# Kernel optimization log

Hardware: AMD Instinct MI355X
Metric: run time of the kernel (lower is better)

Reference implementation:

```python
import jax, jax.numpy as jnp
import numpy as np

EPS = 1e-5

def _bn(x, g, b, axes):
    # training-mode BatchNorm: biased batch stats over `axes`
    mu = jnp.mean(x, axis=axes, keepdims=True)
    var = jnp.var(x, axis=axes, keepdims=True)
    return (x - mu) * jax.lax.rsqrt(var + EPS) * g + b

def setup_inputs() -> dict:
    key = jax.random.key(0)
    ks = jax.random.split(key, 8)
    N, C, T, V = 32, 64, 512, 25
    H, D, BC = 3, 8, 16
    return {
        'x': jax.random.normal(ks[0], (N, C, T, V), jnp.float32),
        'A_topo': jax.random.uniform(ks[1], (H, V, V), jnp.float32),
        'ln_g': jnp.ones((C,), jnp.float32),
        'ln_b': jnp.zeros((C,), jnp.float32),
        'qk_w': jax.random.normal(ks[2], (2 * H * D, C), jnp.float32),
        'qk_b': jnp.zeros((2 * H * D,), jnp.float32),
        'convd_w': jax.random.normal(ks[3], (H, C, C), jnp.float32) * 0.05,
        'convd_b': jnp.zeros((H, C), jnp.float32),
        'sagc_bn_g': jnp.ones((C,), jnp.float32),
        'sagc_bn_b': jnp.zeros((C,), jnp.float32),
        'tcn_w1': jax.random.normal(ks[4], (4, BC, C), jnp.float32) * 0.1,
        'tcn_b1': jnp.zeros((4, BC), jnp.float32),
        'tcn_bn1_g': jnp.ones((4, BC), jnp.float32),
        'tcn_bn1_b': jnp.zeros((4, BC), jnp.float32),
        'tcn_w2': jax.random.normal(ks[5], (2, BC, BC, 5), jnp.float32) * 0.1,
        'tcn_b2': jnp.zeros((2, BC), jnp.float32),
        'tcn_bn2_g': jnp.ones((3, BC), jnp.float32),
        'tcn_bn2_b': jnp.zeros((3, BC), jnp.float32),
    }

def reference(x, A_topo, ln_g, ln_b, qk_w, qk_b, convd_w, convd_b,
              sagc_bn_g, sagc_bn_b, tcn_w1, tcn_b1, tcn_bn1_g, tcn_bn1_b,
              tcn_w2, tcn_b2, tcn_bn2_g, tcn_bn2_b):
    N, C, T, V = x.shape
    H = A_topo.shape[0]
    D = qk_w.shape[0] // (2 * H)
    scale = D ** -0.5

    # ---- SelfAttention ----
    feat = jnp.transpose(x, (0, 2, 3, 1))              # n t v c
    mu = feat.mean(-1, keepdims=True)
    var = feat.var(-1, keepdims=True)
    y = (feat - mu) * jax.lax.rsqrt(var + EPS) * ln_g + ln_b
    qk = y @ qk_w.T + qk_b                             # n t v 2HD
    q, k = jnp.split(qk, 2, axis=-1)
    q = q.reshape(N, T, V, H, D)
    k = k.reshape(N, T, V, H, D)
    dots = jnp.einsum('ntihd,ntjhd->nthij', q, k) * scale
    attn = jax.nn.softmax(dots, axis=-1)               # n t h v v

    # ---- SA_GC ----
    A = attn * A_topo                                  # broadcast (H,V,V)
    z = jnp.einsum('nthij,ntjc->nthic', A, feat)       # per-head A_h @ feature
    sa = jnp.einsum('nthic,hoc->noti', z, convd_w)     # fused per-head 1x1 convs
    sa = sa + convd_b.sum(0)[None, :, None, None]
    sa = _bn(sa, sagc_bn_g[None, :, None, None], sagc_bn_b[None, :, None, None], (0, 2, 3))
    y_gc = jax.nn.relu(sa + x)                         # down = identity (in==out)

    # ---- MultiScale_TemporalConv ----
    pre = jnp.einsum('nctv,koc->nkotv', y_gc, tcn_w1) + tcn_b1[None, :, :, None, None]
    pre = _bn(pre, tcn_bn1_g[None, :, :, None, None], tcn_bn1_b[None, :, :, None, None], (0, 3, 4))
    act = jax.nn.relu(pre[:, :3])                      # branches 0..2 get ReLU
    branches = []
    for i, d in enumerate((1, 2)):                     # dilated temporal convs
        pad = 2 * d                                    # (kernel-1)*d//2
        w = tcn_w2[i][:, :, :, None]                   # (O,I,5,1)
        zb = jax.lax.conv_general_dilated(
            act[:, i], w, (1, 1), ((pad, pad), (0, 0)), rhs_dilation=(d, 1),
            dimension_numbers=('NCHW', 'OIHW', 'NCHW'))
        zb = zb + tcn_b2[i][None, :, None, None]
        zb = _bn(zb, tcn_bn2_g[i][None, :, None, None], tcn_bn2_b[i][None, :, None, None], (0, 2, 3))
        branches.append(zb)
    p = jax.lax.reduce_window(act[:, 2], -jnp.inf, jax.lax.max,
                              (1, 1, 3, 1), (1, 1, 1, 1),
                              ((0, 0), (0, 0), (1, 1), (0, 0)))
    p = _bn(p, tcn_bn2_g[2][None, :, None, None], tcn_bn2_b[2][None, :, None, None], (0, 2, 3))
    branches.append(p)
    branches.append(pre[:, 3])                         # plain 1x1 branch
    tcn_out = jnp.concatenate(branches, axis=1)        # (N, C, T, V)

    # ---- EncodingBlock residual (identity: in==out, stride==1) ----
    return jax.nn.relu(tcn_out + x)
```

## Files before the change

### kernel.cpp

```cpp
#include <hip/hip_runtime.h>


#define EPS 1e-5f

typedef __bf16 bf16;
typedef __bf16 bf16x8 __attribute__((ext_vector_type(8)));
typedef float f32x4 __attribute__((ext_vector_type(4)));

__global__ void kprepack(const float* __restrict__ qk_w, const float* __restrict__ convd_w,
                         const float* __restrict__ w1g,
                         bf16* __restrict__ qkB, bf16* __restrict__ convB, bf16* __restrict__ w1B)
{
  int gid = blockIdx.x * 256 + threadIdx.x;
  if (gid < 384) {
    int lane = gid & 63, f = gid >> 6;
    int nt = f >> 1, ks = f & 1;
    int row = nt * 16 + (lane & 15);
    int col = ks * 32 + ((lane >> 4) * 8);
    const float* src = &qk_w[row * 64 + col];
    bf16* dh = &qkB[(f * 64 + lane) * 8];
    bf16* dl = dh + 3072;
    #pragma unroll
    for (int j = 0; j < 8; j++) {
      float w = src[j];
      bf16 h = (bf16)w;
      dh[j] = h;
      dl[j] = (bf16)(w - (float)h);
    }
  } else if (gid < 1920) {
    int g = gid - 384;
    int lane = g & 63, f = g >> 6;
    int nt = f / 6, ks = f - nt * 6;
    int k0 = ks * 32 + ((lane >> 4) * 8);
    int h = k0 >> 6, c = k0 & 63;
    int o = nt * 16 + (lane & 15);
    const float* src = &convd_w[(h * 64 + o) * 64 + c];
    bf16* d = &convB[(f * 64 + lane) * 8];
    #pragma unroll
    for (int j = 0; j < 8; j++) d[j] = (bf16)src[j];
  } else if (gid < 2432) {
    int g = gid - 1920;
    int lane = g & 63, f = g >> 6;
    int nt = f >> 1, ks = f & 1;
    int ko = nt * 16 + (lane & 15);
    int c0 = ks * 32 + ((lane >> 4) * 8);
    const float* src = &w1g[ko * 64 + c0];
    bf16* dh = &w1B[(f * 64 + lane) * 8];
    bf16* dl = dh + 4096;
    #pragma unroll
    for (int j = 0; j < 8; j++) {
      float w = src[j];
      bf16 h = (bf16)w;
      dh[j] = h;
      dl[j] = (bf16)(w - (float)h);
    }
  }
}

__global__ __launch_bounds__(256, 7)
void k1_sa_sagc(const float* __restrict__ x,
                const float* __restrict__ topo,
                const float* __restrict__ ln_g, const float* __restrict__ ln_b,
                const float* __restrict__ qk_b,
                const bf16* __restrict__ qkB, const bf16* __restrict__ convB,
                const float* __restrict__ convd_b,
                bf16* __restrict__ saB, float* __restrict__ pSum, float* __restrict__ pSq)
{
  const int t = blockIdx.x, n = blockIdx.y, tid = threadIdx.x;
  const int blk = n * 512 + t;
  const int lane = tid & 63, wave = tid >> 6;
  const int rr = lane & 15, co = (lane >> 4) * 8, rq = (lane >> 4) * 4;

  __shared__ __align__(16) float smem[5512];
  bf16*  featT  = (bf16*)smem;
  float* yF     = smem + 1280;
  bf16*  sAttn  = (bf16*)(smem + 1280);
  float* sPartS = smem + 3008;
  float* sPartQ = smem + 3208;
  float* sLnG   = smem + 3408;
  float* sLnB   = smem + 3472;
  float* sQK    = smem + 3008;
  bf16*  zL     = (bf16*)(smem + 3008);

  const int v = tid & 31, cb = tid >> 5;
  float xv[8];
  {
    const float* xp = &x[((n * 64 + cb) * 512 + t) * 25 + (v < 25 ? v : 0)];
    float s = 0.f, q = 0.f;
    #pragma unroll
    for (int k = 0; k < 8; k++) {
      float f = (v < 25) ? xp[k * 102400] : 0.f;
      xv[k] = f;
      featT[(cb + 8 * k) * 40 + v] = (bf16)f;
      s += f; q += f * f;
    }
    s += __shfl_xor(s, 32); q += __shfl_xor(q, 32);
    if (lane < 32 && v < 25) { sPartS[v * 4 + wave] = s; sPartQ[v * 4 + wave] = q; }
    if (tid < 64) { sLnG[tid] = ln_g[tid]; sLnB[tid] = ln_b[tid]; }
    if (tid < 64) {
      #pragma unroll
      for (int j = 25; j < 32; j++) featT[tid * 40 + j] = (bf16)0.f;
    }
  }
  __syncthreads();

  if (v < 25) {
    float S = sPartS[v * 4] + sPartS[v * 4 + 1] + sPartS[v * 4 + 2] + sPartS[v * 4 + 3];
    float Q = sPartQ[v * 4] + sPartQ[v * 4 + 1] + sPartQ[v * 4 + 2] + sPartQ[v * 4 + 3];
    float mu = S * (1.f / 64.f);
    float rstd = rsqrtf(Q * (1.f / 64.f) - mu * mu + EPS);
    #pragma unroll
    for (int k = 0; k < 8; k++) {
      int c = cb + 8 * k;
      yF[v * 69 + c] = (xv[k] - mu) * rstd * sLnG[c] + sLnB[c];
    }
  }
  __syncthreads();

  {
    const int mt = wave & 1;
    const int r0 = mt * 16 + rr;
    bf16x8 Ah[2], Al[2];
    #pragma unroll
    for (int ks = 0; ks < 2; ks++) {
      const float* yp = &yF[r0 * 69 + ks * 32 + co];
      #pragma unroll
      for (int j = 0; j < 8; j++) {
        float yv = yp[j];
        bf16 h = (bf16)yv;
        Ah[ks][j] = h;
        Al[ks][j] = (bf16)(yv - (float)h);
      }
    }
    #pragma unroll
    for (int q = 0; q < 2; q++) {
      if (wave >= 2 && q > 0) break;
      int nt = (wave < 2) ? (q * 2) : 1;
      float qb = qk_b[nt * 16 + rr];
      f32x4 acc = {qb, qb, qb, qb};
      #pragma unroll
      for (int ks = 0; ks < 2; ks++) {
        bf16x8 Bh = *(const bf16x8*)&qkB[((nt * 2 + ks) * 64 + lane) * 8];
        bf16x8 Bl = *(const bf16x8*)&qkB[3072 + ((nt * 2 + ks) * 64 + lane) * 8];
        acc = __builtin_amdgcn_mfma_f32_16x16x32_bf16(Ah[ks], Bh, acc, 0, 0, 0);
        acc = __builtin_amdgcn_mfma_f32_16x16x32_bf16(Ah[ks], Bl, acc, 0, 0, 0);
        acc = __builtin_amdgcn_mfma_f32_16x16x32_bf16(Al[ks], Bh, acc, 0, 0, 0);
      }
      #pragma unroll
      for (int r = 0; r < 4; r++) {
        int i = mt * 16 + rq + r;
        if (i < 25) sQK[i * 56 + nt * 16 + rr] = acc[r];
      }
    }
  }
  __syncthreads();

  if (tid < 150) {
    int p = tid >> 1, half = tid & 1;
    int h = p / 25, i = p - (p / 25) * 25;
    const float* qr = &sQK[i * 56 + h * 8];
    float4 qa = *(const float4*)qr, qb4 = *(const float4*)(qr + 4);
    const int j0 = half * 13;
    const int cnt = 13 - half;
    float lgv[13];
    float lmax = -3.4e38f;
    #pragma unroll
    for (int jj = 0; jj < 13; jj++) {
      int j = j0 + jj; j = j > 24 ? 24 : j;
      const float* kr = &sQK[j * 56 + 24 + h * 8];
      float4 ka = *(const float4*)kr, kb = *(const float4*)(kr + 4);
      float d = qa.x * ka.x + qa.y * ka.y + qa.z * ka.z + qa.w * ka.w
              + qb4.x * kb.x + qb4.y * kb.y + qb4.z * kb.z + qb4.w * kb.w;
      d *= 0.35355339059327373f;
      lgv[jj] = d;
      lmax = fmaxf(lmax, d);
    }
    lmax = fmaxf(lmax, __shfl_xor(lmax, 1));
    float se = 0.f;
    #pragma unroll
    for (int jj = 0; jj < 13; jj++) {
      float e = __expf(lgv[jj] - lmax);
      lgv[jj] = e;
      if (jj < cnt) se += e;
    }
    se += __shfl_xor(se, 1);
    float inv = 1.f / se;
    bf16* ar = &sAttn[(h * 25 + i) * 40];
    #pragma unroll
    for (int jj = 0; jj < 13; jj++) {
      int j = j0 + jj;
      if (jj < cnt) ar[j] = (bf16)(lgv[jj] * inv * topo[(h * 25 + i) * 25 + j]);
    }
    if (half) {
      #pragma unroll
      for (int j = 25; j < 32; j++) ar[j] = (bf16)0.f;
    }
  }
  __syncthreads();

  {
    const int nt = wave;
    bf16x8 Bf = *(const bf16x8*)&featT[(nt * 16 + rr) * 40 + co];
    #pragma unroll
    for (int h = 0; h < 3; h++) {
      #pragma unroll
      for (int mt = 0; mt < 2; mt++) {
        bf16x8 Af = *(const bf16x8*)&sAttn[(h * 25 + mt * 16 + rr) * 40 + co];
        f32x4 az = {0.f, 0.f, 0.f, 0.f};
        az = __builtin_amdgcn_mfma_f32_16x16x32_bf16(Af, Bf, az, 0, 0, 0);
        #pragma unroll
        for (int r = 0; r < 4; r++) {
          int i = mt * 16 + rq + r;
          if (i < 25) zL[i * 200 + h * 64 + nt * 16 + rr] = (bf16)az[r];
        }
      }
    }
  }
  __syncthreads();

  {
    const int nt = wave;
    int o = nt * 16 + rr;
    float cb2 = convd_b[o] + convd_b[64 + o] + convd_b[128 + o];
    float po = 0.f, pq = 0.f;
    #pragma unroll
    for (int mt = 0; mt < 2; mt++) {
      int zr = mt * 16 + rr;
      zr = (zr < 25) ? zr : 0;
      f32x4 acc = {cb2, cb2, cb2, cb2};
      #pragma unroll
      for (int ks = 0; ks < 6; ks++) {
        bf16x8 Az = *(const bf16x8*)&zL[zr * 200 + ks * 32 + co];
        bf16x8 Bw = *(const bf16x8*)&convB[((nt * 6 + ks) * 64 + lane) * 8];
        acc = __builtin_amdgcn_mfma_f32_16x16x32_bf16(Az, Bw, acc, 0, 0, 0);
      }
      #pragma unroll
      for (int r = 0; r < 4; r++) {
        int i = mt * 16 + rq + r;
        if (i < 25) {
          float val = acc[r];
          saB[blk * 1600 + o * 25 + i] = (bf16)val;
          po += val; pq += val * val;
        }
      }
    }
    po += __shfl_xor(po, 16); pq += __shfl_xor(pq, 16);
    po += __shfl_xor(po, 32); pq += __shfl_xor(pq, 32);
    if (lane < 16) {
      pSum[blk * 64 + o] = po;
      pSq [blk * 64 + o] = pq;
    }
  }
}

__global__ __launch_bounds__(256, 8)
void kpart(const float* __restrict__ pS, const float* __restrict__ pQ,
           float* __restrict__ oS, float* __restrict__ oQ)
{
  const int g = blockIdx.x, tid = threadIdx.x;
  const int c = tid & 63, r = tid >> 6;
  float s = 0.f, q = 0.f;
  for (int i = 0; i < 16; i++) {
    int b = g * 64 + r * 16 + i;
    s += pS[b * 64 + c]; q += pQ[b * 64 + c];
  }
  __shared__ float ls[4][64], lq[4][64];
  ls[r][c] = s; lq[r][c] = q;
  __syncthreads();
  if (tid < 64) {
    oS[g * 64 + tid] = ls[0][tid] + ls[1][tid] + ls[2][tid] + ls[3][tid];
    oQ[g * 64 + tid] = lq[0][tid] + lq[1][tid] + lq[2][tid] + lq[3][tid];
  }
}

__global__ __launch_bounds__(256, 4)
void kreduce(const float* __restrict__ pS, const float* __restrict__ pQ,
             int npart, int C, float invN,
             const float* __restrict__ g, const float* __restrict__ bta,
             float* __restrict__ sc, float* __restrict__ sh)
{
  int c = blockIdx.x, tid = threadIdx.x;
  float s = 0.f, q = 0.f;
  for (int i = tid; i < npart; i += 256) { s += pS[i * C + c]; q += pQ[i * C + c]; }
  #pragma unroll
  for (int m = 1; m < 64; m <<= 1) { s += __shfl_xor(s, m); q += __shfl_xor(q, m); }
  __shared__ float rs[4], rq[4];
  int w = tid >> 6;
  if ((tid & 63) == 0) { rs[w] = s; rq[w] = q; }
  __syncthreads();
  if (tid == 0) {
    float S = rs[0] + rs[1] + rs[2] + rs[3];
    float Q = rq[0] + rq[1] + rq[2] + rq[3];
    float mu = S * invN, var = Q * invN - mu * mu;
    float r = rsqrtf(var + EPS);
    sc[c] = g[c] * r;
    sh[c] = bta[c] - mu * g[c] * r;
  }
}

__global__ __launch_bounds__(256, 8)
void k3_ygc_pre(const float* __restrict__ x, const bf16* __restrict__ saB,
                const float* __restrict__ scS, const float* __restrict__ shS,
                const bf16* __restrict__ w1B, const float* __restrict__ b1,
                bf16* __restrict__ preB, float* __restrict__ pSum, float* __restrict__ pSq)
{
  const int t = blockIdx.x, n = blockIdx.y, tid = threadIdx.x;
  const int blk = n * 512 + t;
  const int lane = tid & 63, wave = tid >> 6;
  const int rr = lane & 15, co = (lane >> 4) * 8, rq = (lane >> 4) * 4;

  __shared__ __align__(16) float smem[3656];
  bf16*  yH   = (bf16*)smem;
  bf16*  yL   = (bf16*)(smem + 900);
  float* sPre = smem + 1800;

  if (tid < 200) {
    int lin = tid * 8;
    int c = lin / 25, v = lin - c * 25;
    bf16x8 s8 = *(const bf16x8*)&saB[blk * 1600 + lin];
    #pragma unroll
    for (int e = 0; e < 8; e++) {
      float val = scS[c] * (float)s8[e] + shS[c] + x[((n * 64 + c) * 512 + t) * 25 + v];
      val = fmaxf(val, 0.f);
      bf16 h = (bf16)val;
      yH[v * 72 + c] = h;
      yL[v * 72 + c] = (bf16)(val - (float)h);
      if (++v == 25) { v = 0; c++; }
    }
  }
  __syncthreads();

  {
    const int nt = wave;
    bf16x8 Ah[2][2], Al[2][2];
    #pragma unroll
    for (int mt = 0; mt < 2; mt++) {
      int r0 = mt * 16 + rr;
      #pragma unroll
      for (int ks = 0; ks < 2; ks++) {
        Ah[mt][ks] = *(const bf16x8*)&yH[r0 * 72 + ks * 32 + co];
        Al[mt][ks] = *(const bf16x8*)&yL[r0 * 72 + ks * 32 + co];
      }
    }
    float bb = b1[nt * 16 + rr];
    #pragma unroll
    for (int mt = 0; mt < 2; mt++) {
      f32x4 acc = {bb, bb, bb, bb};
      #pragma unroll
      for (int ks = 0; ks < 2; ks++) {
        bf16x8 Bh = *(const bf16x8*)&w1B[((nt * 2 + ks) * 64 + lane) * 8];
        bf16x8 Bl = *(const bf16x8*)&w1B[4096 + ((nt * 2 + ks) * 64 + lane) * 8];
        acc = __builtin_amdgcn_mfma_f32_16x16x32_bf16(Ah[mt][ks], Bh, acc, 0, 0, 0);
        acc = __builtin_amdgcn_mfma_f32_16x16x32_bf16(Ah[mt][ks], Bl, acc, 0, 0, 0);
        acc = __builtin_amdgcn_mfma_f32_16x16x32_bf16(Al[mt][ks], Bh, acc, 0, 0, 0);
      }
      #pragma unroll
      for (int r = 0; r < 4; r++) {
        int i = mt * 16 + rq + r;
        if (i < 25) sPre[(nt * 16 + rr) * 29 + i] = acc[r];
      }
    }
  }
  __syncthreads();

  if (tid < 200) {
    int lin = tid * 8;
    bf16x8 p8;
    #pragma unroll
    for (int e = 0; e < 8; e++) {
      int q = lin + e, ko = q / 25, v = q - ko * 25;
      p8[e] = (bf16)sPre[ko * 29 + v];
    }
    *(bf16x8*)&preB[blk * 1600 + lin] = p8;
  }
  if (tid < 64) {
    float s = 0.f, q = 0.f;
    #pragma unroll
    for (int i = 0; i < 25; i++) { float v = sPre[tid * 29 + i]; s += v; q += v * v; }
    pSum[blk * 64 + tid] = s;
    pSq [blk * 64 + tid] = q;
  }
}

template<int D>
__device__ __forceinline__ void conv5(const float* __restrict__ sIn, const float* __restrict__ sW,
                                      float4 bias, int o4, int v, int tb, float acc[8][4])
{
  #pragma unroll
  for (int s = 0; s < 8; s++) {
    acc[s][0] = bias.x; acc[s][1] = bias.y; acc[s][2] = bias.z; acc[s][3] = bias.w;
  }
  const int NW = 8 + 4 * D;
  for (int ic = 0; ic < 16; ic++) {
    float4 wk[5];
    #pragma unroll
    for (int kt = 0; kt < 5; kt++) wk[kt] = *(const float4*)&sW[(ic * 5 + kt) * 16 + o4];
    float xw[8 + 4 * D];
    #pragma unroll
    for (int w = 0; w < NW; w++) xw[w] = sIn[(ic * 24 + (tb - 2 * D + w + 4)) * 25 + v];
    #pragma unroll
    for (int s = 0; s < 8; s++)
      #pragma unroll
      for (int kt = 0; kt < 5; kt++) {
        float xv = xw[s + kt * D];
        acc[s][0] += xv * wk[kt].x; acc[s][1] += xv * wk[kt].y;
        acc[s][2] += xv * wk[kt].z; acc[s][3] += xv * wk[kt].w;
      }
  }
}

__global__ __launch_bounds__(256, 3)
void k5_tcn_branch(const bf16* __restrict__ preB,
                   const float* __restrict__ sc1, const float* __restrict__ sh1,
                   const float* __restrict__ w2, const float* __restrict__ b2,
                   bf16* __restrict__ zbB, float* __restrict__ pSum2, float* __restrict__ pSq2)
{
  const int tt = blockIdx.x, b = blockIdx.y, n = blockIdx.z;
  const int tid = threadIdx.x, t0 = tt * 16;
  __shared__ __align__(16) float sIn[16 * 24 * 25];
  __shared__ __align__(16) float sW[16 * 5 * 16];
  __shared__ float sRedS[4][4][4], sRedQ[4][4][4];

  for (int idx = tid; idx < 1200; idx += 256) {
    int r = idx / 50, k8 = idx - r * 50;
    int gt = t0 - 4 + r;
    int lin = k8 * 8;
    if (gt >= 0 && gt < 512) {
      bf16x8 p8 = *(const bf16x8*)&preB[((n * 512 + gt) * 64 + b * 16) * 25 + lin];
      #pragma unroll
      for (int e = 0; e < 8; e++) {
        int q = lin + e, ic = q / 25, v = q - ic * 25;
        int ch = b * 16 + ic;
        sIn[(ic * 24 + r) * 25 + v] = fmaxf(sc1[ch] * (float)p8[e] + sh1[ch], 0.f);
      }
    } else {
      #pragma unroll
      for (int e = 0; e < 8; e++) {
        int q = lin + e, ic = q / 25, v = q - ic * 25;
        sIn[(ic * 24 + r) * 25 + v] = 0.f;
      }
    }
  }
  if (b < 2)
    for (int idx = tid; idx < 1280; idx += 256) {
      int o = idx / 80, rem = idx - o * 80;
      int ic = rem / 5, kt = rem - ic * 5;
      sW[(ic * 5 + kt) * 16 + o] = w2[((b * 16 + o) * 16 + ic) * 5 + kt];
    }
  __syncthreads();

  float po[4] = {0.f, 0.f, 0.f, 0.f}, pq[4] = {0.f, 0.f, 0.f, 0.f};
  if (tid < 200) {
    int tx = tid & 3, o4 = tx * 4;
    int g = tid >> 2;
    int v = g % 25, th = g / 25;
    int tb = th * 8;
    float acc[8][4];
    if (b == 0)      conv5<1>(sIn, sW, *(const float4*)&b2[o4],      o4, v, tb, acc);
    else if (b == 1) conv5<2>(sIn, sW, *(const float4*)&b2[16 + o4], o4, v, tb, acc);
    else {
      #pragma unroll
      for (int s = 0; s < 8; s++)
        #pragma unroll
        for (int j = 0; j < 4; j++) {
          int o = o4 + j, r = tb + s + 4;
          float a = sIn[(o * 24 + r - 1) * 25 + v];
          float m = sIn[(o * 24 + r    ) * 25 + v];
          float c = sIn[(o * 24 + r + 1) * 25 + v];
          acc[s][j] = fmaxf(fmaxf(a, m), c);
        }
    }
    #pragma unroll
    for (int s = 0; s < 8; s++) {
      int gt = t0 + tb + s;
      #pragma unroll
      for (int j = 0; j < 4; j++) {
        float val = acc[s][j];
        zbB[(((b * 32 + n) * 512 + gt) * 16 + (o4 + j)) * 25 + v] = (bf16)val;
        po[j] += val; pq[j] += val * val;
      }
    }
  }
  #pragma unroll
  for (int m = 4; m < 64; m <<= 1) {
    #pragma unroll
    for (int j = 0; j < 4; j++) { po[j] += __shfl_xor(po[j], m); pq[j] += __shfl_xor(pq[j], m); }
  }
  int lane = tid & 63, w = tid >> 6;
  if (lane < 4) {
    #pragma unroll
    for (int j = 0; j < 4; j++) { sRedS[w][lane][j] = po[j]; sRedQ[w][lane][j] = pq[j]; }
  }
  __syncthreads();
  if (tid < 16) {
    int o = tid, txo = o >> 2, j = o & 3;
    float s = 0.f, q = 0.f;
    #pragma unroll
    for (int ww = 0; ww < 4; ww++) { s += sRedS[ww][txo][j]; q += sRedQ[ww][txo][j]; }
    int pidx = (n * 32 + tt) * 48 + b * 16 + o;
    pSum2[pidx] = s; pSq2[pidx] = q;
  }
}

__global__ __launch_bounds__(256, 8)
void k7_final(const float* __restrict__ x, const bf16* __restrict__ preB,
              const bf16* __restrict__ zbB,
              const float* __restrict__ sc1, const float* __restrict__ sh1,
              const float* __restrict__ sc2, const float* __restrict__ sh2,
              float* __restrict__ out)
{
  const int bid = blockIdx.x;
  const int n = bid >> 6, tc = bid & 63;
  const int t0 = tc * 8;
  for (int e = threadIdx.x; e < 12800; e += 256) {
    int ch = e / 200, r = e - ch * 200;
    int tl = r / 25, v = r - tl * 25;
    int t = t0 + tl;
    int b = ch >> 4, o = ch & 15;
    float val;
    if (b < 3) {
      val = sc2[b * 16 + o] * (float)zbB[(((b * 32 + n) * 512 + t) * 16 + o) * 25 + v]
          + sh2[b * 16 + o];
    } else {
      int ko = 48 + o;
      val = sc1[ko] * (float)preB[((n * 512 + t) * 64 + ko) * 25 + v] + sh1[ko];
    }
    int ax = (n * 64 + ch) * 12800 + t * 25 + v;
    out[ax] = fmaxf(val + x[ax], 0.f);
  }
}

extern "C" void kernel_launch(void* const* d_in, const int* in_sizes, int n_in,
                              void* d_out, int out_size, void* d_ws, size_t ws_size,
                              hipStream_t stream)
{
  const float* x       = (const float*)d_in[0];
  const float* topo    = (const float*)d_in[1];
  const float* ln_g    = (const float*)d_in[2];
  const float* ln_b    = (const float*)d_in[3];
  const float* qk_w    = (const float*)d_in[4];
  const float* qk_b    = (const float*)d_in[5];
  const float* convd_w = (const float*)d_in[6];
  const float* convd_b = (const float*)d_in[7];
  const float* sagc_g  = (const float*)d_in[8];
  const float* sagc_b  = (const float*)d_in[9];
  const float* w1      = (const float*)d_in[10];
  const float* b1      = (const float*)d_in[11];
  const float* bn1_g   = (const float*)d_in[12];
  const float* bn1_b   = (const float*)d_in[13];
  const float* w2      = (const float*)d_in[14];
  const float* b2      = (const float*)d_in[15];
  const float* bn2_g   = (const float*)d_in[16];
  const float* bn2_b   = (const float*)d_in[17];
  float* out = (float*)d_out;
  float* ws  = (float*)d_ws;

  bf16*  preB  = (bf16*)ws;
  bf16*  zbB   = (bf16*)(ws + 13107200);
  float* pSum1 = ws + 22937600;
  float* pSq1  = ws + 23986176;
  float* pSum2 = ws + 25034752;
  float* pSq2  = ws + 25083904;
  float* scS   = ws + 25133056;  float* shS = scS + 64;
  float* sc1   = scS + 128;      float* sh1 = scS + 192;
  float* sc2   = scS + 256;      float* sh2 = scS + 304;
  bf16*  qkB   = (bf16*)(ws + 25133440);
  bf16*  convB = (bf16*)(ws + 25136512);
  bf16*  w1B   = (bf16*)(ws + 25142656);
  float* oS1   = ws + 25146752;
  float* oQ1   = ws + 25163136;
  bf16*  saB   = (bf16*)d_out;

  const float invN = 1.f / 409600.f;

  kprepack<<<10, 256, 0, stream>>>(qk_w, convd_w, w1, qkB, convB, w1B);
  k1_sa_sagc<<<dim3(512, 32), 256, 0, stream>>>(x, topo, ln_g, ln_b, qk_b,
                                                qkB, convB, convd_b, saB, pSum1, pSq1);
  kpart<<<256, 256, 0, stream>>>(pSum1, pSq1, oS1, oQ1);
  kreduce<<<64, 256, 0, stream>>>(oS1, oQ1, 256, 64, invN, sagc_g, sagc_b, scS, shS);
  k3_ygc_pre<<<dim3(512, 32), 256, 0, stream>>>(x, saB, scS, shS, w1B, b1,
                                                preB, pSum1, pSq1);
  kpart<<<256, 256, 0, stream>>>(pSum1, pSq1, oS1, oQ1);
  kreduce<<<64, 256, 0, stream>>>(oS1, oQ1, 256, 64, invN, bn1_g, bn1_b, sc1, sh1);
  k5_tcn_branch<<<dim3(32, 3, 32), 256, 0, stream>>>(preB, sc1, sh1, w2, b2,
                                                     zbB, pSum2, pSq2);
  kreduce<<<48, 256, 0, stream>>>(pSum2, pSq2, 1024, 48, invN, bn2_g, bn2_b, sc2, sh2);
  k7_final<<<2048, 256, 0, stream>>>(x, preB, zbB, sc1, sh1, sc2, sh2, out);
}
```

Before: 336.3 us.

## Cache bf16 transposed copy of x for later kernels and halve TCN shared tile

k1 now writes a bf16 copy of x in a [n,t,c,v] layout. k3 and k7 read that copy instead of the fp32 strided x, which cuts DRAM traffic and makes their loads contiguous. The bf16 rounding of the residual adds precision error to the final output. The TCN branch kernel now stages input channels in two halves of 8, halving its shared buffer and raising the occupancy hint from 3 to 6, at the cost of an extra sync round.

```diff
diff --git a/kernel.cpp b/kernel.cpp
--- a/kernel.cpp
+++ b/kernel.cpp
@@ -64,7 +64,8 @@
                 const float* __restrict__ qk_b,
                 const bf16* __restrict__ qkB, const bf16* __restrict__ convB,
                 const float* __restrict__ convd_b,
-                bf16* __restrict__ saB, float* __restrict__ pSum, float* __restrict__ pSq)
+                bf16* __restrict__ saB, bf16* __restrict__ xB,
+                float* __restrict__ pSum, float* __restrict__ pSq)
 {
   const int t = blockIdx.x, n = blockIdx.y, tid = threadIdx.x;
   const int blk = n * 512 + t;
@@ -91,7 +92,9 @@
     for (int k = 0; k < 8; k++) {
       float f = (v < 25) ? xp[k * 102400] : 0.f;
       xv[k] = f;
-      featT[(cb + 8 * k) * 40 + v] = (bf16)f;
+      bf16 fb = (bf16)f;
+      featT[(cb + 8 * k) * 40 + v] = fb;
+      if (v < 25) xB[blk * 1600 + (cb + 8 * k) * 25 + v] = fb;
       s += f; q += f * f;
     }
     s += __shfl_xor(s, 32); q += __shfl_xor(q, 32);
@@ -299,7 +302,7 @@
 }
 
 __global__ __launch_bounds__(256, 8)
-void k3_ygc_pre(const float* __restrict__ x, const bf16* __restrict__ saB,
+void k3_ygc_pre(const bf16* __restrict__ xB, const bf16* __restrict__ saB,
                 const float* __restrict__ scS, const float* __restrict__ shS,
                 const bf16* __restrict__ w1B, const float* __restrict__ b1,
                 bf16* __restrict__ preB, float* __restrict__ pSum, float* __restrict__ pSq)
@@ -318,9 +321,10 @@
     int lin = tid * 8;
     int c = lin / 25, v = lin - c * 25;
     bf16x8 s8 = *(const bf16x8*)&saB[blk * 1600 + lin];
+    bf16x8 x8 = *(const bf16x8*)&xB[blk * 1600 + lin];
     #pragma unroll
     for (int e = 0; e < 8; e++) {
-      float val = scS[c] * (float)s8[e] + shS[c] + x[((n * 64 + c) * 512 + t) * 25 + v];
+      float val = scS[c] * (float)s8[e] + shS[c] + (float)x8[e];
       val = fmaxf(val, 0.f);
       bf16 h = (bf16)val;
       yH[v * 72 + c] = h;
@@ -383,18 +387,16 @@
 }
 
 template<int D>
-__device__ __forceinline__ void conv5(const float* __restrict__ sIn, const float* __restrict__ sW,
-                                      float4 bias, int o4, int v, int tb, float acc[8][4])
-{
-  #pragma unroll
-  for (int s = 0; s < 8; s++) {
-    acc[s][0] = bias.x; acc[s][1] = bias.y; acc[s][2] = bias.z; acc[s][3] = bias.w;
-  }
+__device__ __forceinline__ void conv5_half(const float* __restrict__ sIn,
+                                           const float* __restrict__ sW, int h2,
+                                           int o4, int v, int tb, float acc[8][4])
+{
   const int NW = 8 + 4 * D;
-  for (int ic = 0; ic < 16; ic++) {
+  for (int ic = 0; ic < 8; ic++) {
+    int icg = h2 * 8 + ic;
     float4 wk[5];
     #pragma unroll
-    for (int kt = 0; kt < 5; kt++) wk[kt] = *(const float4*)&sW[(ic * 5 + kt) * 16 + o4];
+    for (int kt = 0; kt < 5; kt++) wk[kt] = *(const float4*)&sW[(icg * 5 + kt) * 16 + o4];
     float xw[8 + 4 * D];
     #pragma unroll
     for (int w = 0; w < NW; w++) xw[w] = sIn[(ic * 24 + (tb - 2 * D + w + 4)) * 25 + v];
@@ -409,7 +411,7 @@
   }
 }
 
-__global__ __launch_bounds__(256, 3)
+__global__ __launch_bounds__(256, 6)
 void k5_tcn_branch(const bf16* __restrict__ preB,
                    const float* __restrict__ sc1, const float* __restrict__ sh1,
                    const float* __restrict__ w2, const float* __restrict__ b2,
@@ -417,59 +419,74 @@
 {
   const int tt = blockIdx.x, b = blockIdx.y, n = blockIdx.z;
   const int tid = threadIdx.x, t0 = tt * 16;
-  __shared__ __align__(16) float sIn[16 * 24 * 25];
+  __shared__ __align__(16) float sIn[8 * 24 * 25];
   __shared__ __align__(16) float sW[16 * 5 * 16];
   __shared__ float sRedS[4][4][4], sRedQ[4][4][4];
 
-  for (int idx = tid; idx < 1200; idx += 256) {
-    int r = idx / 50, k8 = idx - r * 50;
-    int gt = t0 - 4 + r;
-    int lin = k8 * 8;
-    if (gt >= 0 && gt < 512) {
-      bf16x8 p8 = *(const bf16x8*)&preB[((n * 512 + gt) * 64 + b * 16) * 25 + lin];
-      #pragma unroll
-      for (int e = 0; e < 8; e++) {
-        int q = lin + e, ic = q / 25, v = q - ic * 25;
-        int ch = b * 16 + ic;
-        sIn[(ic * 24 + r) * 25 + v] = fmaxf(sc1[ch] * (float)p8[e] + sh1[ch], 0.f);
-      }
-    } else {
-      #pragma unroll
-      for (int e = 0; e < 8; e++) {
-        int q = lin + e, ic = q / 25, v = q - ic * 25;
-        sIn[(ic * 24 + r) * 25 + v] = 0.f;
-      }
-    }
-  }
   if (b < 2)
     for (int idx = tid; idx < 1280; idx += 256) {
       int o = idx / 80, rem = idx - o * 80;
       int ic = rem / 5, kt = rem - ic * 5;
       sW[(ic * 5 + kt) * 16 + o] = w2[((b * 16 + o) * 16 + ic) * 5 + kt];
     }
-  __syncthreads();
+
+  const int tx = tid & 3, o4 = tx * 4;
+  const int g = tid >> 2;
+  const int v = g % 25, th = g / 25;
+  const int tb = th * 8;
+  float acc[8][4];
+  if (tid < 200 && b < 2) {
+    const float* bp = &b2[b * 16 + o4];
+    #pragma unroll
+    for (int s = 0; s < 8; s++) {
+      acc[s][0] = bp[0]; acc[s][1] = bp[1]; acc[s][2] = bp[2]; acc[s][3] = bp[3];
+    }
+  }
+
+  for (int h2 = 0; h2 < 2; h2++) {
+    __syncthreads();
+    for (int idx = tid; idx < 600; idx += 256) {
+      int r = idx / 25, k8 = idx - r * 25;
+      int gt = t0 - 4 + r;
+      int lin = k8 * 8;
+      if (gt >= 0 && gt < 512) {
+        bf16x8 p8 = *(const bf16x8*)&preB[((n * 512 + gt) * 64 + b * 16 + h2 * 8) * 25 + lin];
+        #pragma unroll
+        for (int e = 0; e < 8; e++) {
+          int q = lin + e, ic = q / 25, vv = q - ic * 25;
+          int ch = b * 16 + h2 * 8 + ic;
+          sIn[(ic * 24 + r) * 25 + vv] = fmaxf(sc1[ch] * (float)p8[e] + sh1[ch], 0.f);
+        }
+      } else {
+        #pragma unroll
+        for (int e = 0; e < 8; e++) {
+          int q = lin + e, ic = q / 25, vv = q - ic * 25;
+          sIn[(ic * 24 + r) * 25 + vv] = 0.f;
+        }
+      }
+    }
+    __syncthreads();
+    if (tid < 200) {
+      if (b == 0)      conv5_half<1>(sIn, sW, h2, o4, v, tb, acc);
+      else if (b == 1) conv5_half<2>(sIn, sW, h2, o4, v, tb, acc);
+      else if ((o4 >> 3) == h2) {
+        int ob = o4 & 7;
+        #pragma unroll
+        for (int s = 0; s < 8; s++)
+          #pragma unroll
+          for (int j = 0; j < 4; j++) {
+            int o = ob + j, r = tb + s + 4;
+            float a = sIn[(o * 24 + r - 1) * 25 + v];
+            float m = sIn[(o * 24 + r    ) * 25 + v];
+            float c = sIn[(o * 24 + r + 1) * 25 + v];
+            acc[s][j] = fmaxf(fmaxf(a, m), c);
+          }
+      }
+    }
+  }
 
   float po[4] = {0.f, 0.f, 0.f, 0.f}, pq[4] = {0.f, 0.f, 0.f, 0.f};
   if (tid < 200) {
-    int tx = tid & 3, o4 = tx * 4;
-    int g = tid >> 2;
-    int v = g % 25, th = g / 25;
-    int tb = th * 8;
-    float acc[8][4];
-    if (b == 0)      conv5<1>(sIn, sW, *(const float4*)&b2[o4],      o4, v, tb, acc);
-    else if (b == 1) conv5<2>(sIn, sW, *(const float4*)&b2[16 + o4], o4, v, tb, acc);
-    else {
-      #pragma unroll
-      for (int s = 0; s < 8; s++)
-        #pragma unroll
-        for (int j = 0; j < 4; j++) {
-          int o = o4 + j, r = tb + s + 4;
-          float a = sIn[(o * 24 + r - 1) * 25 + v];
-          float m = sIn[(o * 24 + r    ) * 25 + v];
-          float c = sIn[(o * 24 + r + 1) * 25 + v];
-          acc[s][j] = fmaxf(fmaxf(a, m), c);
-        }
-    }
     #pragma unroll
     for (int s = 0; s < 8; s++) {
       int gt = t0 + tb + s;
@@ -503,7 +520,7 @@
 }
 
 __global__ __launch_bounds__(256, 8)
-void k7_final(const float* __restrict__ x, const bf16* __restrict__ preB,
+void k7_final(const bf16* __restrict__ xB, const bf16* __restrict__ preB,
               const bf16* __restrict__ zbB,
               const float* __restrict__ sc1, const float* __restrict__ sh1,
               const float* __restrict__ sc2, const float* __restrict__ sh2,
@@ -525,8 +542,9 @@
       int ko = 48 + o;
       val = sc1[ko] * (float)preB[((n * 512 + t) * 64 + ko) * 25 + v] + sh1[ko];
     }
+    float xr = (float)xB[(n * 512 + t) * 1600 + ch * 25 + v];
     int ax = (n * 64 + ch) * 12800 + t * 25 + v;
-    out[ax] = fmaxf(val + x[ax], 0.f);
+    out[ax] = fmaxf(val + xr, 0.f);
   }
 }
 
@@ -569,21 +587,22 @@
   bf16*  w1B   = (bf16*)(ws + 25142656);
   float* oS1   = ws + 25146752;
   float* oQ1   = ws + 25163136;
+  bf16*  xB    = (bf16*)(ws + 25179520);
   bf16*  saB   = (bf16*)d_out;
 
   const float invN = 1.f / 409600.f;
 
   kprepack<<<10, 256, 0, stream>>>(qk_w, convd_w, w1, qkB, convB, w1B);
   k1_sa_sagc<<<dim3(512, 32), 256, 0, stream>>>(x, topo, ln_g, ln_b, qk_b,
-                                                qkB, convB, convd_b, saB, pSum1, pSq1);
+                                                qkB, convB, convd_b, saB, xB, pSum1, pSq1);
   kpart<<<256, 256, 0, stream>>>(pSum1, pSq1, oS1, oQ1);
   kreduce<<<64, 256, 0, stream>>>(oS1, oQ1, 256, 64, invN, sagc_g, sagc_b, scS, shS);
-  k3_ygc_pre<<<dim3(512, 32), 256, 0, stream>>>(x, saB, scS, shS, w1B, b1,
+  k3_ygc_pre<<<dim3(512, 32), 256, 0, stream>>>(xB, saB, scS, shS, w1B, b1,
                                                 preB, pSum1, pSq1);
   kpart<<<256, 256, 0, stream>>>(pSum1, pSq1, oS1, oQ1);
   kreduce<<<64, 256, 0, stream>>>(oS1, oQ1, 256, 64, invN, bn1_g, bn1_b, sc1, sh1);
   k5_tcn_branch<<<dim3(32, 3, 32), 256, 0, stream>>>(preB, sc1, sh1, w2, b2,
                                                      zbB, pSum2, pSq2);
   kreduce<<<48, 256, 0, stream>>>(pSum2, pSq2, 1024, 48, invN, bn2_g, bn2_b, sc2, sh2);
-  k7_final<<<2048, 256, 0, stream>>>(x, preB, zbB, sc1, sh1, sc2, sh2, out);
-}
+  k7_final<<<2048, 256, 0, stream>>>(xB, preB, zbB, sc1, sh1, sc2, sh2, out);
+}
```

Result: slower. 403.0 us (+19.8%).

## Process eight timesteps per block with register prefetch of next inputs

Applied to the files above, without the earlier changes.

Both k1_sa_sagc and k3_ygc_pre now loop over 8 consecutive timesteps per block instead of one. Each iteration prefetches the next timestep's x (and saB) into registers before the barrier, so global load latency overlaps with compute. LayerNorm gamma/beta are kept in registers rather than shared memory. The grid shrinks eightfold (2048 blocks), so there is less block launch overhead but also less parallelism, more registers live per thread, and a serial dependency chain inside each block.

```diff
diff --git a/kernel.cpp b/kernel.cpp
--- a/kernel.cpp
+++ b/kernel.cpp
@@ -66,8 +66,7 @@
                 const float* __restrict__ convd_b,
                 bf16* __restrict__ saB, float* __restrict__ pSum, float* __restrict__ pSq)
 {
-  const int t = blockIdx.x, n = blockIdx.y, tid = threadIdx.x;
-  const int blk = n * 512 + t;
+  const int tc = blockIdx.x, n = blockIdx.y, tid = threadIdx.x;
   const int lane = tid & 63, wave = tid >> 6;
   const int rr = lane & 15, co = (lane >> 4) * 8, rq = (lane >> 4) * 4;
 
@@ -77,178 +76,198 @@
   bf16*  sAttn  = (bf16*)(smem + 1280);
   float* sPartS = smem + 3008;
   float* sPartQ = smem + 3208;
-  float* sLnG   = smem + 3408;
-  float* sLnB   = smem + 3472;
   float* sQK    = smem + 3008;
   bf16*  zL     = (bf16*)(smem + 3008);
 
   const int v = tid & 31, cb = tid >> 5;
+
+  float lng[8], lnb[8];
+  #pragma unroll
+  for (int k = 0; k < 8; k++) { lng[k] = ln_g[cb + 8 * k]; lnb[k] = ln_b[cb + 8 * k]; }
+
   float xv[8];
   {
-    const float* xp = &x[((n * 64 + cb) * 512 + t) * 25 + (v < 25 ? v : 0)];
-    float s = 0.f, q = 0.f;
-    #pragma unroll
-    for (int k = 0; k < 8; k++) {
-      float f = (v < 25) ? xp[k * 102400] : 0.f;
-      xv[k] = f;
-      featT[(cb + 8 * k) * 40 + v] = (bf16)f;
-      s += f; q += f * f;
-    }
-    s += __shfl_xor(s, 32); q += __shfl_xor(q, 32);
-    if (lane < 32 && v < 25) { sPartS[v * 4 + wave] = s; sPartQ[v * 4 + wave] = q; }
-    if (tid < 64) { sLnG[tid] = ln_g[tid]; sLnB[tid] = ln_b[tid]; }
-    if (tid < 64) {
-      #pragma unroll
-      for (int j = 25; j < 32; j++) featT[tid * 40 + j] = (bf16)0.f;
-    }
-  }
-  __syncthreads();
-
-  if (v < 25) {
-    float S = sPartS[v * 4] + sPartS[v * 4 + 1] + sPartS[v * 4 + 2] + sPartS[v * 4 + 3];
-    float Q = sPartQ[v * 4] + sPartQ[v * 4 + 1] + sPartQ[v * 4 + 2] + sPartQ[v * 4 + 3];
-    float mu = S * (1.f / 64.f);
-    float rstd = rsqrtf(Q * (1.f / 64.f) - mu * mu + EPS);
-    #pragma unroll
-    for (int k = 0; k < 8; k++) {
-      int c = cb + 8 * k;
-      yF[v * 69 + c] = (xv[k] - mu) * rstd * sLnG[c] + sLnB[c];
-    }
-  }
-  __syncthreads();
-
-  {
-    const int mt = wave & 1;
-    const int r0 = mt * 16 + rr;
-    bf16x8 Ah[2], Al[2];
-    #pragma unroll
-    for (int ks = 0; ks < 2; ks++) {
-      const float* yp = &yF[r0 * 69 + ks * 32 + co];
-      #pragma unroll
-      for (int j = 0; j < 8; j++) {
-        float yv = yp[j];
-        bf16 h = (bf16)yv;
-        Ah[ks][j] = h;
-        Al[ks][j] = (bf16)(yv - (float)h);
-      }
-    }
-    #pragma unroll
-    for (int q = 0; q < 2; q++) {
-      if (wave >= 2 && q > 0) break;
-      int nt = (wave < 2) ? (q * 2) : 1;
-      float qb = qk_b[nt * 16 + rr];
-      f32x4 acc = {qb, qb, qb, qb};
+    const float* xp = &x[((n * 64 + cb) * 512 + tc * 8) * 25 + (v < 25 ? v : 0)];
+    #pragma unroll
+    for (int k = 0; k < 8; k++) xv[k] = (v < 25) ? xp[k * 102400] : 0.f;
+  }
+
+  #pragma unroll 1
+  for (int tl = 0; tl < 8; tl++) {
+    const int t = tc * 8 + tl;
+    const int blk = n * 512 + t;
+
+    {
+      float s = 0.f, q = 0.f;
+      #pragma unroll
+      for (int k = 0; k < 8; k++) {
+        float f = xv[k];
+        featT[(cb + 8 * k) * 40 + v] = (bf16)f;
+        s += f; q += f * f;
+      }
+      s += __shfl_xor(s, 32); q += __shfl_xor(q, 32);
+      if (lane < 32 && v < 25) { sPartS[v * 4 + wave] = s; sPartQ[v * 4 + wave] = q; }
+    }
+    float xn[8];
+    if (tl < 7) {
+      const float* xp = &x[((n * 64 + cb) * 512 + t + 1) * 25 + (v < 25 ? v : 0)];
+      #pragma unroll
+      for (int k = 0; k < 8; k++) xn[k] = (v < 25) ? xp[k * 102400] : 0.f;
+    }
+    __syncthreads();
+
+    if (v < 25) {
+      float S = sPartS[v * 4] + sPartS[v * 4 + 1] + sPartS[v * 4 + 2] + sPartS[v * 4 + 3];
+      float Q = sPartQ[v * 4] + sPartQ[v * 4 + 1] + sPartQ[v * 4 + 2] + sPartQ[v * 4 + 3];
+      float mu = S * (1.f / 64.f);
+      float rstd = rsqrtf(Q * (1.f / 64.f) - mu * mu + EPS);
+      #pragma unroll
+      for (int k = 0; k < 8; k++) {
+        int c = cb + 8 * k;
+        yF[v * 69 + c] = (xv[k] - mu) * rstd * lng[k] + lnb[k];
+      }
+    }
+    __syncthreads();
+
+    {
+      const int mt = wave & 1;
+      const int r0 = mt * 16 + rr;
+      bf16x8 Ah[2], Al[2];
       #pragma unroll
       for (int ks = 0; ks < 2; ks++) {
-        bf16x8 Bh = *(const bf16x8*)&qkB[((nt * 2 + ks) * 64 + lane) * 8];
-        bf16x8 Bl = *(const bf16x8*)&qkB[3072 + ((nt * 2 + ks) * 64 + lane) * 8];
-        acc = __builtin_amdgcn_mfma_f32_16x16x32_bf16(Ah[ks], Bh, acc, 0, 0, 0);
-        acc = __builtin_amdgcn_mfma_f32_16x16x32_bf16(Ah[ks], Bl, acc, 0, 0, 0);
-        acc = __builtin_amdgcn_mfma_f32_16x16x32_bf16(Al[ks], Bh, acc, 0, 0, 0);
-      }
-      #pragma unroll
-      for (int r = 0; r < 4; r++) {
-        int i = mt * 16 + rq + r;
-        if (i < 25) sQK[i * 56 + nt * 16 + rr] = acc[r];
-      }
-    }
-  }
-  __syncthreads();
-
-  if (tid < 150) {
-    int p = tid >> 1, half = tid & 1;
-    int h = p / 25, i = p - (p / 25) * 25;
-    const float* qr = &sQK[i * 56 + h * 8];
-    float4 qa = *(const float4*)qr, qb4 = *(const float4*)(qr + 4);
-    const int j0 = half * 13;
-    const int cnt = 13 - half;
-    float lgv[13];
-    float lmax = -3.4e38f;
-    #pragma unroll
-    for (int jj = 0; jj < 13; jj++) {
-      int j = j0 + jj; j = j > 24 ? 24 : j;
-      const float* kr = &sQK[j * 56 + 24 + h * 8];
-      float4 ka = *(const float4*)kr, kb = *(const float4*)(kr + 4);
-      float d = qa.x * ka.x + qa.y * ka.y + qa.z * ka.z + qa.w * ka.w
-              + qb4.x * kb.x + qb4.y * kb.y + qb4.z * kb.z + qb4.w * kb.w;
-      d *= 0.35355339059327373f;
-      lgv[jj] = d;
-      lmax = fmaxf(lmax, d);
-    }
-    lmax = fmaxf(lmax, __shfl_xor(lmax, 1));
-    float se = 0.f;
-    #pragma unroll
-    for (int jj = 0; jj < 13; jj++) {
-      float e = __expf(lgv[jj] - lmax);
-      lgv[jj] = e;
-      if (jj < cnt) se += e;
-    }
-    se += __shfl_xor(se, 1);
-    float inv = 1.f / se;
-    bf16* ar = &sAttn[(h * 25 + i) * 40];
-    #pragma unroll
-    for (int jj = 0; jj < 13; jj++) {
-      int j = j0 + jj;
-      if (jj < cnt) ar[j] = (bf16)(lgv[jj] * inv * topo[(h * 25 + i) * 25 + j]);
-    }
-    if (half) {
-      #pragma unroll
-      for (int j = 25; j < 32; j++) ar[j] = (bf16)0.f;
-    }
-  }
-  __syncthreads();
-
-  {
-    const int nt = wave;
-    bf16x8 Bf = *(const bf16x8*)&featT[(nt * 16 + rr) * 40 + co];
-    #pragma unroll
-    for (int h = 0; h < 3; h++) {
-      #pragma unroll
-      for (int mt = 0; mt < 2; mt++) {
-        bf16x8 Af = *(const bf16x8*)&sAttn[(h * 25 + mt * 16 + rr) * 40 + co];
-        f32x4 az = {0.f, 0.f, 0.f, 0.f};
-        az = __builtin_amdgcn_mfma_f32_16x16x32_bf16(Af, Bf, az, 0, 0, 0);
+        const float* yp = &yF[r0 * 69 + ks * 32 + co];
+        #pragma unroll
+        for (int j = 0; j < 8; j++) {
+          float yv = yp[j];
+          bf16 h = (bf16)yv;
+          Ah[ks][j] = h;
+          Al[ks][j] = (bf16)(yv - (float)h);
+        }
+      }
+      #pragma unroll
+      for (int q = 0; q < 2; q++) {
+        if (wave >= 2 && q > 0) break;
+        int nt = (wave < 2) ? (q * 2) : 1;
+        float qb = qk_b[nt * 16 + rr];
+        f32x4 acc = {qb, qb, qb, qb};
+        #pragma unroll
+        for (int ks = 0; ks < 2; ks++) {
+          bf16x8 Bh = *(const bf16x8*)&qkB[((nt * 2 + ks) * 64 + lane) * 8];
+          bf16x8 Bl = *(const bf16x8*)&qkB[3072 + ((nt * 2 + ks) * 64 + lane) * 8];
+          acc = __builtin_amdgcn_mfma_f32_16x16x32_bf16(Ah[ks], Bh, acc, 0, 0, 0);
+          acc = __builtin_amdgcn_mfma_f32_16x16x32_bf16(Ah[ks], Bl, acc, 0, 0, 0);
+          acc = __builtin_amdgcn_mfma_f32_16x16x32_bf16(Al[ks], Bh, acc, 0, 0, 0);
+        }
         #pragma unroll
         for (int r = 0; r < 4; r++) {
           int i = mt * 16 + rq + r;
-          if (i < 25) zL[i * 200 + h * 64 + nt * 16 + rr] = (bf16)az[r];
-        }
-      }
-    }
-  }
-  __syncthreads();
-
-  {
-    const int nt = wave;
-    int o = nt * 16 + rr;
-    float cb2 = convd_b[o] + convd_b[64 + o] + convd_b[128 + o];
-    float po = 0.f, pq = 0.f;
-    #pragma unroll
-    for (int mt = 0; mt < 2; mt++) {
-      int zr = mt * 16 + rr;
-      zr = (zr < 25) ? zr : 0;
-      f32x4 acc = {cb2, cb2, cb2, cb2};
-      #pragma unroll
-      for (int ks = 0; ks < 6; ks++) {
-        bf16x8 Az = *(const bf16x8*)&zL[zr * 200 + ks * 32 + co];
-        bf16x8 Bw = *(const bf16x8*)&convB[((nt * 6 + ks) * 64 + lane) * 8];
-        acc = __builtin_amdgcn_mfma_f32_16x16x32_bf16(Az, Bw, acc, 0, 0, 0);
-      }
-      #pragma unroll
-      for (int r = 0; r < 4; r++) {
-        int i = mt * 16 + rq + r;
-        if (i < 25) {
-          float val = acc[r];
-          saB[blk * 1600 + o * 25 + i] = (bf16)val;
-          po += val; pq += val * val;
-        }
-      }
-    }
-    po += __shfl_xor(po, 16); pq += __shfl_xor(pq, 16);
-    po += __shfl_xor(po, 32); pq += __shfl_xor(pq, 32);
-    if (lane < 16) {
-      pSum[blk * 64 + o] = po;
-      pSq [blk * 64 + o] = pq;
+          if (i < 25) sQK[i * 56 + nt * 16 + rr] = acc[r];
+        }
+      }
+    }
+    __syncthreads();
+
+    if (tid < 150) {
+      int p = tid >> 1, half = tid & 1;
+      int h = p / 25, i = p - (p / 25) * 25;
+      const float* qr = &sQK[i * 56 + h * 8];
+      float4 qa = *(const float4*)qr, qb4 = *(const float4*)(qr + 4);
+      const int j0 = half * 13;
+      const int cnt = 13 - half;
+      float lgv[13];
+      float lmax = -3.4e38f;
+      #pragma unroll
+      for (int jj = 0; jj < 13; jj++) {
+        int j = j0 + jj; j = j > 24 ? 24 : j;
+        const float* kr = &sQK[j * 56 + 24 + h * 8];
+        float4 ka = *(const float4*)kr, kb = *(const float4*)(kr + 4);
+        float d = qa.x * ka.x + qa.y * ka.y + qa.z * ka.z + qa.w * ka.w
+                + qb4.x * kb.x + qb4.y * kb.y + qb4.z * kb.z + qb4.w * kb.w;
+        d *= 0.35355339059327373f;
+        lgv[jj] = d;
+        lmax = fmaxf(lmax, d);
+      }
+      lmax = fmaxf(lmax, __shfl_xor(lmax, 1));
+      float se = 0.f;
+      #pragma unroll
+      for (int jj = 0; jj < 13; jj++) {
+        float e = __expf(lgv[jj] - lmax);
+        lgv[jj] = e;
+        if (jj < cnt) se += e;
+      }
+      se += __shfl_xor(se, 1);
+      float inv = 1.f / se;
+      bf16* ar = &sAttn[(h * 25 + i) * 40];
+      #pragma unroll
+      for (int jj = 0; jj < 13; jj++) {
+        int j = j0 + jj;
+        if (jj < cnt) ar[j] = (bf16)(lgv[jj] * inv * topo[(h * 25 + i) * 25 + j]);
+      }
+      if (half) {
+        #pragma unroll
+        for (int j = 25; j < 32; j++) ar[j] = (bf16)0.f;
+      }
+    }
+    __syncthreads();
+
+    {
+      const int nt = wave;
+      bf16x8 Bf = *(const bf16x8*)&featT[(nt * 16 + rr) * 40 + co];
+      #pragma unroll
+      for (int h = 0; h < 3; h++) {
+        #pragma unroll
+        for (int mt = 0; mt < 2; mt++) {
+          bf16x8 Af = *(const bf16x8*)&sAttn[(h * 25 + mt * 16 + rr) * 40 + co];
+          f32x4 az = {0.f, 0.f, 0.f, 0.f};
+          az = __builtin_amdgcn_mfma_f32_16x16x32_bf16(Af, Bf, az, 0, 0, 0);
+          #pragma unroll
+          for (int r = 0; r < 4; r++) {
+            int i = mt * 16 + rq + r;
+            if (i < 25) zL[i * 200 + h * 64 + nt * 16 + rr] = (bf16)az[r];
+          }
+        }
+      }
+    }
+    __syncthreads();
+
+    {
+      const int nt = wave;
+      int o = nt * 16 + rr;
+      float cb2 = convd_b[o] + convd_b[64 + o] + convd_b[128 + o];
+      float po = 0.f, pq = 0.f;
+      #pragma unroll
+      for (int mt = 0; mt < 2; mt++) {
+        int zr = mt * 16 + rr;
+        zr = (zr < 25) ? zr : 0;
+        f32x4 acc = {cb2, cb2, cb2, cb2};
+        #pragma unroll
+        for (int ks = 0; ks < 6; ks++) {
+          bf16x8 Az = *(const bf16x8*)&zL[zr * 200 + ks * 32 + co];
+          bf16x8 Bw = *(const bf16x8*)&convB[((nt * 6 + ks) * 64 + lane) * 8];
+          acc = __builtin_amdgcn_mfma_f32_16x16x32_bf16(Az, Bw, acc, 0, 0, 0);
+        }
+        #pragma unroll
+        for (int r = 0; r < 4; r++) {
+          int i = mt * 16 + rq + r;
+          if (i < 25) {
+            float val = acc[r];
+            saB[blk * 1600 + o * 25 + i] = (bf16)val;
+            po += val; pq += val * val;
+          }
+        }
+      }
+      po += __shfl_xor(po, 16); pq += __shfl_xor(pq, 16);
+      po += __shfl_xor(po, 32); pq += __shfl_xor(pq, 32);
+      if (lane < 16) {
+        pSum[blk * 64 + o] = po;
+        pSq [blk * 64 + o] = pq;
+      }
+    }
+    __syncthreads();
+
+    if (tl < 7) {
+      #pragma unroll
+      for (int k = 0; k < 8; k++) xv[k] = xn[k];
     }
   }
 }
@@ -304,8 +323,7 @@
                 const bf16* __restrict__ w1B, const float* __restrict__ b1,
                 bf16* __restrict__ preB, float* __restrict__ pSum, float* __restrict__ pSq)
 {
-  const int t = blockIdx.x, n = blockIdx.y, tid = threadIdx.x;
-  const int blk = n * 512 + t;
+  const int tc = blockIdx.x, n = blockIdx.y, tid = threadIdx.x;
   const int lane = tid & 63, wave = tid >> 6;
   const int rr = lane & 15, co = (lane >> 4) * 8, rq = (lane >> 4) * 4;
 
@@ -314,71 +332,108 @@
   bf16*  yL   = (bf16*)(smem + 900);
   float* sPre = smem + 1800;
 
+  const int lin = (tid < 200) ? tid * 8 : 0;
+  const int c0 = lin / 25, v0 = lin - c0 * 25;
+
+  bf16x8 s8 = {};
+  float x8[8];
   if (tid < 200) {
-    int lin = tid * 8;
-    int c = lin / 25, v = lin - c * 25;
-    bf16x8 s8 = *(const bf16x8*)&saB[blk * 1600 + lin];
+    int blk0 = n * 512 + tc * 8;
+    s8 = *(const bf16x8*)&saB[blk0 * 1600 + lin];
+    int c = c0, v = v0;
     #pragma unroll
     for (int e = 0; e < 8; e++) {
-      float val = scS[c] * (float)s8[e] + shS[c] + x[((n * 64 + c) * 512 + t) * 25 + v];
-      val = fmaxf(val, 0.f);
-      bf16 h = (bf16)val;
-      yH[v * 72 + c] = h;
-      yL[v * 72 + c] = (bf16)(val - (float)h);
+      x8[e] = x[((n * 64 + c) * 512 + tc * 8) * 25 + v];
       if (++v == 25) { v = 0; c++; }
     }
   }
-  __syncthreads();
-
-  {
-    const int nt = wave;
-    bf16x8 Ah[2][2], Al[2][2];
-    #pragma unroll
-    for (int mt = 0; mt < 2; mt++) {
-      int r0 = mt * 16 + rr;
-      #pragma unroll
-      for (int ks = 0; ks < 2; ks++) {
-        Ah[mt][ks] = *(const bf16x8*)&yH[r0 * 72 + ks * 32 + co];
-        Al[mt][ks] = *(const bf16x8*)&yL[r0 * 72 + ks * 32 + co];
-      }
-    }
-    float bb = b1[nt * 16 + rr];
-    #pragma unroll
-    for (int mt = 0; mt < 2; mt++) {
-      f32x4 acc = {bb, bb, bb, bb};
-      #pragma unroll
-      for (int ks = 0; ks < 2; ks++) {
-        bf16x8 Bh = *(const bf16x8*)&w1B[((nt * 2 + ks) * 64 + lane) * 8];
-        bf16x8 Bl = *(const bf16x8*)&w1B[4096 + ((nt * 2 + ks) * 64 + lane) * 8];
-        acc = __builtin_amdgcn_mfma_f32_16x16x32_bf16(Ah[mt][ks], Bh, acc, 0, 0, 0);
-        acc = __builtin_amdgcn_mfma_f32_16x16x32_bf16(Ah[mt][ks], Bl, acc, 0, 0, 0);
-        acc = __builtin_amdgcn_mfma_f32_16x16x32_bf16(Al[mt][ks], Bh, acc, 0, 0, 0);
-      }
-      #pragma unroll
-      for (int r = 0; r < 4; r++) {
-        int i = mt * 16 + rq + r;
-        if (i < 25) sPre[(nt * 16 + rr) * 29 + i] = acc[r];
-      }
-    }
-  }
-  __syncthreads();
-
-  if (tid < 200) {
-    int lin = tid * 8;
-    bf16x8 p8;
-    #pragma unroll
-    for (int e = 0; e < 8; e++) {
-      int q = lin + e, ko = q / 25, v = q - ko * 25;
-      p8[e] = (bf16)sPre[ko * 29 + v];
-    }
-    *(bf16x8*)&preB[blk * 1600 + lin] = p8;
-  }
-  if (tid < 64) {
-    float s = 0.f, q = 0.f;
-    #pragma unroll
-    for (int i = 0; i < 25; i++) { float v = sPre[tid * 29 + i]; s += v; q += v * v; }
-    pSum[blk * 64 + tid] = s;
-    pSq [blk * 64 + tid] = q;
+
+  #pragma unroll 1
+  for (int tl = 0; tl < 8; tl++) {
+    const int t = tc * 8 + tl;
+    const int blk = n * 512 + t;
+
+    if (tid < 200) {
+      int c = c0, v = v0;
+      #pragma unroll
+      for (int e = 0; e < 8; e++) {
+        float val = scS[c] * (float)s8[e] + shS[c] + x8[e];
+        val = fmaxf(val, 0.f);
+        bf16 h = (bf16)val;
+        yH[v * 72 + c] = h;
+        yL[v * 72 + c] = (bf16)(val - (float)h);
+        if (++v == 25) { v = 0; c++; }
+      }
+    }
+    bf16x8 s8n = {};
+    float x8n[8];
+    if (tl < 7 && tid < 200) {
+      s8n = *(const bf16x8*)&saB[(blk + 1) * 1600 + lin];
+      int c = c0, v = v0;
+      #pragma unroll
+      for (int e = 0; e < 8; e++) {
+        x8n[e] = x[((n * 64 + c) * 512 + t + 1) * 25 + v];
+        if (++v == 25) { v = 0; c++; }
+      }
+    }
+    __syncthreads();
+
+    {
+      const int nt = wave;
+      bf16x8 Ah[2][2], Al[2][2];
+      #pragma unroll
+      for (int mt = 0; mt < 2; mt++) {
+        int r0 = mt * 16 + rr;
+        #pragma unroll
+        for (int ks = 0; ks < 2; ks++) {
+          Ah[mt][ks] = *(const bf16x8*)&yH[r0 * 72 + ks * 32 + co];
+          Al[mt][ks] = *(const bf16x8*)&yL[r0 * 72 + ks * 32 + co];
+        }
+      }
+      float bb = b1[nt * 16 + rr];
+      #pragma unroll
+      for (int mt = 0; mt < 2; mt++) {
+        f32x4 acc = {bb, bb, bb, bb};
+        #pragma unroll
+        for (int ks = 0; ks < 2; ks++) {
+          bf16x8 Bh = *(const bf16x8*)&w1B[((nt * 2 + ks) * 64 + lane) * 8];
+          bf16x8 Bl = *(const bf16x8*)&w1B[4096 + ((nt * 2 + ks) * 64 + lane) * 8];
+          acc = __builtin_amdgcn_mfma_f32_16x16x32_bf16(Ah[mt][ks], Bh, acc, 0, 0, 0);
+          acc = __builtin_amdgcn_mfma_f32_16x16x32_bf16(Ah[mt][ks], Bl, acc, 0, 0, 0);
+          acc = __builtin_amdgcn_mfma_f32_16x16x32_bf16(Al[mt][ks], Bh, acc, 0, 0, 0);
+        }
+        #pragma unroll
+        for (int r = 0; r < 4; r++) {
+          int i = mt * 16 + rq + r;
+          if (i < 25) sPre[(nt * 16 + rr) * 29 + i] = acc[r];
+        }
+      }
+    }
+    __syncthreads();
+
+    if (tid < 200) {
+      bf16x8 p8;
+      int ko = c0, v = v0;
+      #pragma unroll
+      for (int e = 0; e < 8; e++) {
+        p8[e] = (bf16)sPre[ko * 29 + v];
+        if (++v == 25) { v = 0; ko++; }
+      }
+      *(bf16x8*)&preB[blk * 1600 + lin] = p8;
+    }
+    if (tid < 64) {
+      float s = 0.f, q = 0.f;
+      #pragma unroll
+      for (int i = 0; i < 25; i++) { float vv = sPre[tid * 29 + i]; s += vv; q += vv * vv; }
+      pSum[blk * 64 + tid] = s;
+      pSq [blk * 64 + tid] = q;
+    }
+
+    if (tl < 7 && tid < 200) {
+      s8 = s8n;
+      #pragma unroll
+      for (int e = 0; e < 8; e++) x8[e] = x8n[e];
+    }
   }
 }
 
@@ -574,12 +629,12 @@
   const float invN = 1.f / 409600.f;
 
   kprepack<<<10, 256, 0, stream>>>(qk_w, convd_w, w1, qkB, convB, w1B);
-  k1_sa_sagc<<<dim3(512, 32), 256, 0, stream>>>(x, topo, ln_g, ln_b, qk_b,
-                                                qkB, convB, convd_b, saB, pSum1, pSq1);
+  k1_sa_sagc<<<dim3(64, 32), 256, 0, stream>>>(x, topo, ln_g, ln_b, qk_b,
+                                               qkB, convB, convd_b, saB, pSum1, pSq1);
   kpart<<<256, 256, 0, stream>>>(pSum1, pSq1, oS1, oQ1);
   kreduce<<<64, 256, 0, stream>>>(oS1, oQ1, 256, 64, invN, sagc_g, sagc_b, scS, shS);
-  k3_ygc_pre<<<dim3(512, 32), 256, 0, stream>>>(x, saB, scS, shS, w1B, b1,
-                                                preB, pSum1, pSq1);
+  k3_ygc_pre<<<dim3(64, 32), 256, 0, stream>>>(x, saB, scS, shS, w1B, b1,
+                                               preB, pSum1, pSq1);
   kpart<<<256, 256, 0, stream>>>(pSum1, pSq1, oS1, oQ1);
   kreduce<<<64, 256, 0, stream>>>(oS1, oQ1, 256, 64, invN, bn1_g, bn1_b, sc1, sh1);
   k5_tcn_branch<<<dim3(32, 3, 32), 256, 0, stream>>>(preB, sc1, sh1, w2, b2,
```

Measured after the change: 782.9 us, median of 2. 133% more time.
